# Performance work log

Hardware: AMD Instinct MI355X
Metric: run time of the kernel (lower is better)

The kernel has to match this reference:

```python
import jax, jax.numpy as jnp
import numpy as np

LN_EPS = 1e-5
CLAMP = 1e-8


def _linear(x, W, b):
    return x @ W + b


def _layernorm(x, g, b):
    mu = x.mean(-1, keepdims=True)
    var = ((x - mu) ** 2).mean(-1, keepdims=True)
    return (x - mu) / jnp.sqrt(var + LN_EPS) * g + b


def _residual(x, W1, b1, W2, b2):
    return jax.nn.relu(_linear(jax.nn.relu(_linear(x, W1, b1)), W2, b2)) + x


def _forward(node_emb, attn_Wq, attn_bq, attn_Wk, attn_bk, attn_Wv, attn_bv,
             attn_Wd, attn_bd, attn_ln_g, attn_ln_b,
             mlp_r1_w1, mlp_r1_b1, mlp_r1_w2, mlp_r1_b2,
             mlp_r2_w1, mlp_r2_b1, mlp_r2_w2, mlp_r2_b2,
             mlp_out_w, mlp_out_b,
             log_phi_r0, log_phi_r1h, log_phi_r1v, log_phi_r2, r0_idx, n):
    x = node_emb  # [1, n^2, D]
    L = attn_Wq.shape[0]
    for l in range(L):  # mask in the original is all zeros -> plain softmax attention
        q = _linear(x, attn_Wq[l], attn_bq[l])
        k = _linear(x, attn_Wk[l], attn_bk[l])
        v = _linear(x, attn_Wv[l], attn_bv[l])
        probs = jax.nn.softmax(jnp.einsum('bqd,bkd->bqk', q, k), axis=-1)
        ctx = jnp.einsum('bqk,bkd->bqd', probs, v)
        x = _layernorm(_linear(ctx, attn_Wd[l], attn_bd[l]) + x, attn_ln_g[l], attn_ln_b[l])
    x0 = x[0]                                  # [n^2, D]
    feats = x0[r0_idx].reshape(r0_idx.shape[0], -1)  # [R0, 4D]
    h = _residual(feats, mlp_r1_w1, mlp_r1_b1, mlp_r1_w2, mlp_r1_b2)
    h = _residual(h, mlp_r2_w1, mlp_r2_b1, mlp_r2_w2, mlp_r2_b2)
    logits = _linear(h, mlp_out_w, mlp_out_b)  # [R0, 16]
    beliefs = jax.nn.softmax(logits, axis=-1).reshape(-1, 2, 2, 2, 2)

    m = n - 1  # plaquettes per row
    # --- R1 horizontal interior edges (row r in 1..n-2, col c in 0..n-2) ---
    r, c = np.meshgrid(np.arange(1, n - 1), np.arange(m), indexing='ij')
    above = ((r - 1) * m + c).ravel()
    below = (r * m + c).ravel()
    h_stack = jnp.stack([beliefs[above].sum((1, 2)),   # edge nodes at plaquette pos 2,3
                         beliefs[below].sum((3, 4))])  # edge nodes at plaquette pos 0,1
    h_bel = h_stack.mean(0)                            # [Eh,2,2]
    mism = jnp.sum((h_stack - h_bel) ** 2)
    # --- R1 vertical interior edges (row r in 0..n-2, col c in 1..n-2) ---
    r, c = np.meshgrid(np.arange(m), np.arange(1, n - 1), indexing='ij')
    left = (r * m + (c - 1)).ravel()
    right = (r * m + c).ravel()
    v_stack = jnp.stack([beliefs[left].sum((1, 3)),    # edge nodes at pos 1,3
                         beliefs[right].sum((2, 4))])  # edge nodes at pos 0,2
    v_bel = v_stack.mean(0)                            # [Ev,2,2]
    mism = mism + jnp.sum((v_stack - v_bel) ** 2)
    # --- R2 interior nodes (r, c in 1..n-2), parents are the 4 incident edges ---
    r, c = np.meshgrid(np.arange(1, n - 1), np.arange(1, n - 1), indexing='ij')
    hl = ((r - 1) * m + (c - 1)).ravel()
    hr = ((r - 1) * m + c).ravel()
    vu = ((r - 1) * (n - 2) + (c - 1)).ravel()
    vd = (r * (n - 2) + (c - 1)).ravel()
    n_stack = jnp.stack([h_bel[hl].sum(1), h_bel[hr].sum(2),
                         v_bel[vu].sum(1), v_bel[vd].sum(2)])
    n_bel = n_stack.mean(0)                            # [V,2]
    mism = mism + jnp.sum((n_stack - n_bel) ** 2)

    # --- Kikuchi energy: counts +1 (plaquette), -1 (edge), +1 (node); log_phi detached ---
    def reg_energy(b, lphi, cnt):
        bc = jnp.maximum(b, CLAMP)
        return cnt * jnp.sum(bc * (jnp.log(bc) - jax.lax.stop_gradient(lphi)))

    energy = (reg_energy(beliefs, log_phi_r0, 1.0)
              + reg_energy(h_bel, log_phi_r1h, -1.0)
              + reg_energy(v_bel, log_phi_r1v, -1.0)
              + reg_energy(n_bel, log_phi_r2, 1.0))
    return energy, mism


def setup_inputs() -> dict:
    n, D, L, HID, OUT = 64, 256, 2, 1024, 16
    m = n - 1
    R0, E, V = m * m, (n - 2) * m, (n - 2) * (n - 2)
    key = jax.random.key(0)
    ks = jax.random.split(key, 24)
    norm = lambda k, sh, s=0.05: jax.random.normal(k, sh, dtype=jnp.float32) * s
    r, c = np.meshgrid(np.arange(m), np.arange(m), indexing='ij')
    i = (r * n + c).ravel()
    r0_idx = jnp.asarray(np.stack([i, i + 1, i + n, i + n + 1], 1), dtype=jnp.int32)
    inp = {
        'node_emb': jax.random.normal(ks[0], (1, n * n, D), dtype=jnp.float32),
        'attn_Wq': norm(ks[1], (L, D, D)), 'attn_bq': jnp.zeros((L, D), jnp.float32),
        'attn_Wk': norm(ks[2], (L, D, D)), 'attn_bk': jnp.zeros((L, D), jnp.float32),
        'attn_Wv': norm(ks[3], (L, D, D)), 'attn_bv': jnp.zeros((L, D), jnp.float32),
        'attn_Wd': norm(ks[4], (L, D, D)), 'attn_bd': jnp.zeros((L, D), jnp.float32),
        'attn_ln_g': jnp.ones((L, D), jnp.float32), 'attn_ln_b': jnp.zeros((L, D), jnp.float32),
        'mlp_r1_w1': norm(ks[5], (HID, HID), 0.03), 'mlp_r1_b1': jnp.zeros((HID,), jnp.float32),
        'mlp_r1_w2': norm(ks[6], (HID, HID), 0.03), 'mlp_r1_b2': jnp.zeros((HID,), jnp.float32),
        'mlp_r2_w1': norm(ks[7], (HID, HID), 0.03), 'mlp_r2_b1': jnp.zeros((HID,), jnp.float32),
        'mlp_r2_w2': norm(ks[8], (HID, HID), 0.03), 'mlp_r2_b2': jnp.zeros((HID,), jnp.float32),
        'mlp_out_w': norm(ks[9], (HID, OUT), 0.03), 'mlp_out_b': jnp.zeros((OUT,), jnp.float32),
        'log_phi_r0': jax.random.normal(ks[10], (R0, 2, 2, 2, 2), dtype=jnp.float32),
        'log_phi_r1h': jax.random.normal(ks[11], (E, 2, 2), dtype=jnp.float32),
        'log_phi_r1v': jax.random.normal(ks[12], (E, 2, 2), dtype=jnp.float32),
        'log_phi_r2': jax.random.normal(ks[13], (V, 2), dtype=jnp.float32),
        'r0_idx': r0_idx,
        'n': n,
    }
    return inp


def reference(node_emb, attn_Wq, attn_bq, attn_Wk, attn_bk, attn_Wv, attn_bv,
              attn_Wd, attn_bd, attn_ln_g, attn_ln_b,
              mlp_r1_w1, mlp_r1_b1, mlp_r1_w2, mlp_r1_b2,
              mlp_r2_w1, mlp_r2_b1, mlp_r2_w2, mlp_r2_b2,
              mlp_out_w, mlp_out_b,
              log_phi_r0, log_phi_r1h, log_phi_r1v, log_phi_r2, r0_idx, n):
    return _forward(node_emb, attn_Wq, attn_bq, attn_Wk, attn_bk, attn_Wv, attn_bv,
                    attn_Wd, attn_bd, attn_ln_g, attn_ln_b,
                    mlp_r1_w1, mlp_r1_b1, mlp_r1_w2, mlp_r1_b2,
                    mlp_r2_w1, mlp_r2_b1, mlp_r2_w2, mlp_r2_b2,
                    mlp_out_w, mlp_out_b,
                    log_phi_r0, log_phi_r1h, log_phi_r1v, log_phi_r2, r0_idx, n)
```

## Files before the change

### kernel.cpp

```cpp
#include <hip/hip_runtime.h>
#include <hip/hip_bf16.h>
#include <math.h>

#define D_    256
#define NSQ   4096
#define NL    2
#define HID_  1024
#define R0_   3969
#define EH_   3906
#define EV_   3906
#define NV_   3844
#define LN_EPS_ 1e-5f
#define CLAMP_  1e-8f
#define TK_    64

typedef float f32x4 __attribute__((ext_vector_type(4)));
typedef __bf16 bf16x8 __attribute__((ext_vector_type(8)));
typedef unsigned short u16x8 __attribute__((ext_vector_type(8)));

__device__ __forceinline__ void gload_lds16(const void* g, void* l) {
    __builtin_amdgcn_global_load_lds(
        (const __attribute__((address_space(1))) void*)g,
        (__attribute__((address_space(3))) void*)l, 16, 0, 0);
}

template<int BM, int BN>
__device__ __forceinline__ void gemm_body(
    const __hip_bfloat16* __restrict__ A, const __hip_bfloat16* __restrict__ Bt,
    const float* __restrict__ bias,
    const float* __restrict__ resf, const __hip_bfloat16* __restrict__ resb,
    void* __restrict__ C, int M, int N, int K, int relu, int outmode,
    int bx, int by)
{
    constexpr int WR  = BM / 64;
    constexpr int WC  = 4 / WR;
    constexpr int WNT = BN / WC;
    constexpr int NF  = WNT / 16;
    constexpr int ACH = BM / 64;
    constexpr int BCH = BN / 64;
    constexpr int ASZ = BM * 32;

    __shared__ __hip_bfloat16 sm[2][(BM + BN) * 32];

    const int t = threadIdx.x;
    const int lane = t & 63, wave = t >> 6;
    const int ln = lane & 15, lg = lane >> 4;
    const int wr = (WR == 1) ? 0 : (wave >> 1);
    const int wc = (WR == 1) ? wave : (wave & 1);
    const int row0 = bx * BM, col0 = by * BN;

    int aoff[ACH], boff[BCH];
    #pragma unroll
    for (int c = 0; c < ACH; ++c) {
        int e = (c * 256 + t) * 8;
        int row = e >> 5, slot = (e >> 3) & 3;
        int kg = slot ^ (row & 3) ^ ((row >> 2) & 3);
        aoff[c] = row * K + kg * 8;
    }
    #pragma unroll
    for (int c = 0; c < BCH; ++c) {
        int e = (c * 256 + t) * 8;
        int row = e >> 5, slot = (e >> 3) & 3;
        int kg = slot ^ (row & 3) ^ ((row >> 2) & 3);
        boff[c] = row * K + kg * 8;
    }
    const int sw = (ln & 3) ^ ((ln >> 2) & 3);

    const __hip_bfloat16* Ab = A + (size_t)row0 * K;
    const __hip_bfloat16* Bb = Bt + (size_t)col0 * K;

    f32x4 acc[4][NF];
    #pragma unroll
    for (int m = 0; m < 4; ++m)
        #pragma unroll
        for (int n = 0; n < NF; ++n) acc[m][n] = f32x4{0.f, 0.f, 0.f, 0.f};

    auto STAGE = [&](int k0, int buf) {
        #pragma unroll
        for (int c = 0; c < ACH; ++c)
            gload_lds16(Ab + k0 + aoff[c], (char*)&sm[buf][0] + (c * 256 + t) * 16);
        #pragma unroll
        for (int c = 0; c < BCH; ++c)
            gload_lds16(Bb + k0 + boff[c], (char*)&sm[buf][ASZ] + (c * 256 + t) * 16);
    };

    STAGE(0, 0);
    __syncthreads();
    int cur = 0;
    for (int k0 = 0; k0 < K; k0 += 32) {
        if (k0 + 32 < K) STAGE(k0 + 32, cur ^ 1);
        bf16x8 af[4], bfr[NF];
        #pragma unroll
        for (int m = 0; m < 4; ++m)
            af[m] = *(const bf16x8*)((const char*)&sm[cur][0] +
                     (size_t)(wr * 64 + m * 16 + ln) * 64 + ((lg ^ sw) << 4));
        #pragma unroll
        for (int n = 0; n < NF; ++n)
            bfr[n] = *(const bf16x8*)((const char*)&sm[cur][ASZ] +
                     (size_t)(wc * WNT + n * 16 + ln) * 64 + ((lg ^ sw) << 4));
        #pragma unroll
        for (int m = 0; m < 4; ++m)
            #pragma unroll
            for (int n = 0; n < NF; ++n)
                acc[m][n] = __builtin_amdgcn_mfma_f32_16x16x32_bf16(
                    af[m], bfr[n], acc[m][n], 0, 0, 0);
        __syncthreads();
        cur ^= 1;
    }

    #pragma unroll
    for (int m = 0; m < 4; ++m) {
        const int rowb = row0 + wr * 64 + m * 16 + lg * 4;
        #pragma unroll
        for (int n = 0; n < NF; ++n) {
            const int col = col0 + wc * WNT + n * 16 + ln;
            const float bv = bias ? bias[col] : 0.f;
            if (outmode == 2) {
                union { ushort4 u4; __hip_bfloat16 h[4]; } pk;
                #pragma unroll
                for (int r = 0; r < 4; ++r) {
                    float v = acc[m][n][r] + bv;
                    if (relu) v = fmaxf(v, 0.f);
                    pk.h[r] = __float2bfloat16(v);
                }
                *(ushort4*)((__hip_bfloat16*)C + (size_t)col * M + rowb) = pk.u4;
            } else if (outmode == 3) {
                union { ushort4 u4; __hip_bfloat16 h[4]; } pk;
                #pragma unroll
                for (int r = 0; r < 4; ++r) {
                    float v = acc[m][n][r] + bv;
                    if (relu) v = fmaxf(v, 0.f);
                    pk.h[r] = __float2bfloat16(v);
                }
                size_t off = ((size_t)((rowb >> 5) * 16 + (col >> 4)) << 9)
                           + (size_t)(((rowb >> 3) & 3) * 16 + (col & 15)) * 8
                           + (rowb & 7);
                *(ushort4*)((__hip_bfloat16*)C + off) = pk.u4;
            } else {
                #pragma unroll
                for (int r = 0; r < 4; ++r) {
                    float v = acc[m][n][r] + bv;
                    if (relu) v = fmaxf(v, 0.f);
                    const size_t idx = (size_t)(rowb + r) * N + col;
                    if (resf) v += resf[idx];
                    if (resb) v += __bfloat162float(resb[idx]);
                    if (outmode == 0) ((float*)C)[idx] = v;
                    else ((__hip_bfloat16*)C)[idx] = __float2bfloat16(v);
                }
            }
        }
    }
}

template<int BM, int BN>
__global__ __launch_bounds__(256) void gemm_t(
    const __hip_bfloat16* __restrict__ A, const __hip_bfloat16* __restrict__ Bt,
    const float* __restrict__ bias,
    const float* __restrict__ resf, const __hip_bfloat16* __restrict__ resb,
    void* __restrict__ C, int M, int N, int K, int relu, int outmode)
{
    gemm_body<BM, BN>(A, Bt, bias, resf, resb, C, M, N, K, relu, outmode,
                      blockIdx.x, blockIdx.y);
}

__global__ __launch_bounds__(256) void gemm_qkv(
    const __hip_bfloat16* __restrict__ xb,
    const __hip_bfloat16* __restrict__ wqkt2, const __hip_bfloat16* __restrict__ wvt2,
    const float* __restrict__ bqk2, const float* __restrict__ bv,
    __hip_bfloat16* __restrict__ qkb, __hip_bfloat16* __restrict__ vf, int l)
{
    const __hip_bfloat16* Bt;
    const float* bias;
    void* C;
    int N, outmode, by;
    if (blockIdx.y < 8) {
        Bt = wqkt2 + (size_t)l * 131072; bias = bqk2 + l * 512;
        C = qkb; N = 512; outmode = 1; by = blockIdx.y;
    } else {
        Bt = wvt2 + (size_t)l * 65536; bias = bv + l * D_;
        C = vf; N = D_; outmode = 3; by = blockIdx.y - 8;
    }
    gemm_body<64, 64>(xb, Bt, bias, nullptr, nullptr, C, NSQ, N, D_, 0, outmode,
                      blockIdx.x, by);
}

__global__ __launch_bounds__(256) void gemm_n16b(
    const __hip_bfloat16* __restrict__ A, const __hip_bfloat16* __restrict__ Bt,
    const float* __restrict__ bias, const float* __restrict__ lphi0,
    float* __restrict__ beliefs, float* __restrict__ out, int M, int K)
{
    const int t = threadIdx.x, lane = t & 63, wave = t >> 6;
    const int ln = lane & 15, lg = lane >> 4;
    const int r0 = blockIdx.x * 64 + wave * 16;
    f32x4 acc = {0.f, 0.f, 0.f, 0.f};
    for (int k0 = 0; k0 < K; k0 += 32) {
        bf16x8 a = *(const bf16x8*)(A + (size_t)(r0 + ln) * K + k0 + lg * 8);
        bf16x8 b = *(const bf16x8*)(Bt + (size_t)ln * K + k0 + lg * 8);
        acc = __builtin_amdgcn_mfma_f32_16x16x32_bf16(a, b, acc, 0, 0, 0);
    }
    float e = 0.f;
    #pragma unroll
    for (int r = 0; r < 4; ++r) {
        const int row = r0 + lg * 4 + r;
        float v = acc[r] + bias[ln];
        float mx = v;
        mx = fmaxf(mx, __shfl_xor(mx, 1));
        mx = fmaxf(mx, __shfl_xor(mx, 2));
        mx = fmaxf(mx, __shfl_xor(mx, 4));
        mx = fmaxf(mx, __shfl_xor(mx, 8));
        float ex = __expf(v - mx);
        float s = ex;
        s += __shfl_xor(s, 1);
        s += __shfl_xor(s, 2);
        s += __shfl_xor(s, 4);
        s += __shfl_xor(s, 8);
        if (row < R0_) {
            float bb = ex / s;
            beliefs[(size_t)row * 16 + ln] = bb;
            float bc = fmaxf(bb, CLAMP_);
            e += bc * (logf(bc) - lphi0[(size_t)row * 16 + ln]);
        }
    }
    #pragma unroll
    for (int off = 32; off; off >>= 1) e += __shfl_down(e, off);
    if (lane == 0) atomicAdd(&out[0], e);
}

__global__ __launch_bounds__(256) void prep_k(
    const float* __restrict__ node_emb, __hip_bfloat16* __restrict__ xb,
    const float* __restrict__ outw, __hip_bfloat16* __restrict__ outwt,
    const float* __restrict__ Wq, const float* __restrict__ Wk,
    const float* __restrict__ Wv, const float* __restrict__ Wd,
    __hip_bfloat16* __restrict__ wqkt2, __hip_bfloat16* __restrict__ wvt2,
    __hip_bfloat16* __restrict__ wdt2,
    const float* __restrict__ bq, const float* __restrict__ bk,
    float* __restrict__ bqk2,
    const float* __restrict__ M0, const float* __restrict__ M1,
    const float* __restrict__ M2, const float* __restrict__ M3,
    __hip_bfloat16* __restrict__ T0, __hip_bfloat16* __restrict__ T1,
    __hip_bfloat16* __restrict__ T2, __hip_bfloat16* __restrict__ T3)
{
    __shared__ float tile[32][33];
    const int b = blockIdx.x, t = threadIdx.x;
    if (b < 1024) {
        int p = b * 256 + t;
        float4 v = *(const float4*)(node_emb + (size_t)p * 4);
        union { ushort4 u4; __hip_bfloat16 h[4]; } pk;
        pk.h[0] = __float2bfloat16(v.x); pk.h[1] = __float2bfloat16(v.y);
        pk.h[2] = __float2bfloat16(v.z); pk.h[3] = __float2bfloat16(v.w);
        *(ushort4*)(xb + (size_t)p * 4) = pk.u4;
    } else if (b < 1088) {
        int i = (b - 1024) * 256 + t;
        int n = i >> 10, k = i & 1023;
        outwt[i] = __float2bfloat16(outw[k * 16 + n]);
    } else if (b < 1600) {
        int idx = b - 1088;
        int z = idx >> 6, bx = (idx >> 3) & 7, by = idx & 7;
        int l = z >> 2, w = z & 3;
        const float* W = (w == 0 ? Wq : w == 1 ? Wk : w == 2 ? Wv : Wd) + (size_t)l * 65536;
        __hip_bfloat16* Wt = w == 0 ? wqkt2 + (size_t)l * 131072
                           : w == 1 ? wqkt2 + (size_t)l * 131072 + 65536
                           : w == 2 ? wvt2 + (size_t)l * 65536
                                    : wdt2 + (size_t)l * 65536;
        int k0 = bx * 32, n0 = by * 32;
        int r = t >> 3, c4 = (t & 7) * 4;
        float4 v = *(const float4*)(W + (size_t)(k0 + r) * 256 + n0 + c4);
        tile[r][c4 + 0] = v.x; tile[r][c4 + 1] = v.y;
        tile[r][c4 + 2] = v.z; tile[r][c4 + 3] = v.w;
        __syncthreads();
        union { ushort4 u4; __hip_bfloat16 h[4]; } pk;
        #pragma unroll
        for (int i = 0; i < 4; ++i) pk.h[i] = __float2bfloat16(tile[c4 + i][r]);
        *(ushort4*)(Wt + (size_t)(n0 + r) * 256 + k0 + c4) = pk.u4;
    } else if (b < 1604) {
        int idx = (b - 1600) * 256 + t;
        int l = idx >> 9, j = idx & 511;
        bqk2[idx] = j < 256 ? bq[l * 256 + j] : bk[l * 256 + j - 256];
    } else {
        int idx = b - 1604;
        int z = idx >> 10, rem = idx & 1023;
        const float* W = z == 0 ? M0 : z == 1 ? M1 : z == 2 ? M2 : M3;
        __hip_bfloat16* Wt = z == 0 ? T0 : z == 1 ? T1 : z == 2 ? T2 : T3;
        int k0 = (rem >> 5) * 32, n0 = (rem & 31) * 32;
        int r = t >> 3, c4 = (t & 7) * 4;
        float4 v = *(const float4*)(W + (size_t)(k0 + r) * 1024 + n0 + c4);
        tile[r][c4 + 0] = v.x; tile[r][c4 + 1] = v.y;
        tile[r][c4 + 2] = v.z; tile[r][c4 + 3] = v.w;
        __syncthreads();
        union { ushort4 u4; __hip_bfloat16 h[4]; } pk;
        #pragma unroll
        for (int i = 0; i < 4; ++i) pk.h[i] = __float2bfloat16(tile[c4 + i][r]);
        *(ushort4*)(Wt + (size_t)(n0 + r) * 1024 + k0 + c4) = pk.u4;
    }
}

template<int KS>
__global__ __launch_bounds__(512, 2) void attn_mfma_t(
    const __hip_bfloat16* __restrict__ qk, const __hip_bfloat16* __restrict__ vf,
    __hip_bfloat16* __restrict__ po, float* __restrict__ pm, float* __restrict__ pl)
{
    constexpr int KRANGE = NSQ / KS;
    constexpr int NT = KRANGE / TK_;
    constexpr int VOFF = 65536;
    constexpr int POFF = 98304;
    const int t = threadIdx.x;
    const int wave = t >> 6, lane = t & 63;
    const int ln = lane & 15, lg = lane >> 4;
    const int q0 = blockIdx.x * 128 + wave * 16;
    const int ks = blockIdx.y;
    const int k0 = ks * KRANGE;

    __shared__ __align__(16) char smem[116736];

    bf16x8 qa[8];
    #pragma unroll
    for (int s = 0; s < 8; ++s)
        qa[s] = *(const bf16x8*)(qk + (size_t)(q0 + ln) * 512 + s * 32 + lg * 8);

    int srcoff[4];
    #pragma unroll
    for (int c = 0; c < 4; ++c) {
        int row = c * 16 + (t >> 5);
        int g = (t & 31) ^ ((row & 15) << 1);
        srcoff[c] = row * 512 + 256 + g * 8;
    }
    int rb[8];
    #pragma unroll
    for (int s8 = 0; s8 < 8; ++s8)
        rb[s8] = ln * 512 + (((s8 * 4 + lg) ^ (ln << 1)) << 4);

    f32x4 o[16];
    #pragma unroll
    for (int nt = 0; nt < 16; ++nt) o[nt] = f32x4{0.f, 0.f, 0.f, 0.f};
    float rm = -1e30f, rl = 0.f;

    {
        const __hip_bfloat16* src = qk + (size_t)k0 * 512;
        #pragma unroll
        for (int c = 0; c < 4; ++c)
            gload_lds16(src + srcoff[c], smem + c * 8192 + t * 16);
    }
    __syncthreads();

    for (int it = 0; it < NT; ++it) {
        const int cur = it & 1;
        {
            const __hip_bfloat16* vsrc = vf + ((size_t)((k0 + it * TK_) >> 5) << 13);
            #pragma unroll
            for (int c = 0; c < 4; ++c) {
                int idx = c * 512 + t;
                gload_lds16(vsrc + (size_t)idx * 8, smem + VOFF + idx * 16);
            }
        }
        {
            const int itn = (it + 1 < NT) ? it + 1 : it;
            const __hip_bfloat16* src = qk + (size_t)(k0 + itn * TK_) * 512;
            #pragma unroll
            for (int c = 0; c < 4; ++c)
                gload_lds16(src + srcoff[c], smem + (cur ^ 1) * 32768 + c * 8192 + t * 16);
        }
        const char* kbase = smem + cur * 32768;
        f32x4 s4[4];
        #pragma unroll
        for (int nt = 0; nt < 4; ++nt) {
            f32x4 acc = {0.f, 0.f, 0.f, 0.f};
            #pragma unroll
            for (int s8 = 0; s8 < 8; ++s8) {
                bf16x8 kb = *(const bf16x8*)(kbase + nt * 8192 + rb[s8]);
                acc = __builtin_amdgcn_mfma_f32_16x16x32_bf16(kb, qa[s8], acc, 0, 0, 0);
            }
            s4[nt] = acc;
        }
        float mx = -1e30f;
        #pragma unroll
        for (int nt = 0; nt < 4; ++nt)
            #pragma unroll
            for (int r = 0; r < 4; ++r) mx = fmaxf(mx, s4[nt][r]);
        mx = fmaxf(mx, __shfl_xor(mx, 16));
        mx = fmaxf(mx, __shfl_xor(mx, 32));
        float sc = 1.f;
        if (__any(mx > rm + 8.f)) {
            float mnew = fmaxf(rm, mx);
            sc = __expf(rm - mnew);
            rm = mnew;
            float scr[4];
            #pragma unroll
            for (int r = 0; r < 4; ++r) scr[r] = __shfl(sc, lg * 4 + r);
            #pragma unroll
            for (int nt = 0; nt < 16; ++nt)
                #pragma unroll
                for (int r = 0; r < 4; ++r) o[nt][r] *= scr[r];
        }
        float rs = 0.f;
        #pragma unroll
        for (int nt = 0; nt < 4; ++nt)
            #pragma unroll
            for (int r = 0; r < 4; ++r) {
                float p = __expf(s4[nt][r] - rm);
                s4[nt][r] = p;
                rs += p;
            }
        rs += __shfl_xor(rs, 16);
        rs += __shfl_xor(rs, 32);
        rl = rl * sc + rs;
        char* prow = smem + POFF + wave * 2304 + ln * 144;
        #pragma unroll
        for (int nt = 0; nt < 4; ++nt) {
            union { ushort4 u4; __hip_bfloat16 h[4]; } pk;
            #pragma unroll
            for (int r = 0; r < 4; ++r) pk.h[r] = __float2bfloat16(s4[nt][r]);
            *(ushort4*)(prow + nt * 32 + lg * 8) = pk.u4;
        }
        asm volatile("s_waitcnt lgkmcnt(0)" ::: "memory");
        __builtin_amdgcn_sched_barrier(0);
        bf16x8 pa0 = *(const bf16x8*)(prow + lg * 16);
        bf16x8 pa1 = *(const bf16x8*)(prow + 64 + lg * 16);
        asm volatile("s_waitcnt vmcnt(4)" ::: "memory");
        __builtin_amdgcn_sched_barrier(0);
        __builtin_amdgcn_s_barrier();
        const char* vl = smem + VOFF;
        #pragma unroll
        for (int ntd = 0; ntd < 16; ++ntd) {
            bf16x8 vb0 = *(const bf16x8*)(vl + ntd * 1024 + lane * 16);
            bf16x8 vb1 = *(const bf16x8*)(vl + 16384 + ntd * 1024 + lane * 16);
            o[ntd] = __builtin_amdgcn_mfma_f32_16x16x32_bf16(pa0, vb0, o[ntd], 0, 0, 0);
            o[ntd] = __builtin_amdgcn_mfma_f32_16x16x32_bf16(pa1, vb1, o[ntd], 0, 0, 0);
        }
        __syncthreads();
    }
    unsigned short* ob = (unsigned short*)(smem + wave * 8448);
    #pragma unroll
    for (int nt = 0; nt < 16; ++nt)
        #pragma unroll
        for (int r = 0; r < 4; ++r) {
            __hip_bfloat16 h = __float2bfloat16(o[nt][r]);
            ob[(lg * 4 + r) * 264 + nt * 16 + ln] = *(unsigned short*)&h;
        }
    asm volatile("s_waitcnt lgkmcnt(0)" ::: "memory");
    __builtin_amdgcn_sched_barrier(0);
    unsigned short* pob = (unsigned short*)po;
    #pragma unroll
    for (int i = 0; i < 8; ++i) {
        int f = i * 64 + lane;
        int row = f >> 5, dc = f & 31;
        u16x8 vv = *(const u16x8*)(ob + row * 264 + dc * 8);
        *(u16x8*)(pob + ((size_t)ks * NSQ + q0 + row) * D_ + dc * 8) = vv;
    }
    if (lane < 16) {
        pm[ks * NSQ + q0 + lane] = rm;
        pl[ks * NSQ + q0 + lane] = rl;
    }
}

template<int KS>
__global__ __launch_bounds__(256) void attn_combine_t(
    const __hip_bfloat16* __restrict__ po, const float* __restrict__ pm,
    const float* __restrict__ pl, __hip_bfloat16* __restrict__ ctx)
{
    const int idx8 = blockIdx.x * 256 + threadIdx.x;
    const int row = idx8 >> 5;
    float m[KS], ms = -1e30f;
    #pragma unroll
    for (int s = 0; s < KS; ++s) { m[s] = pm[s * NSQ + row]; ms = fmaxf(ms, m[s]); }
    float l = 0.f, w[KS];
    #pragma unroll
    for (int s = 0; s < KS; ++s) {
        w[s] = __expf(m[s] - ms);
        l += w[s] * pl[s * NSQ + row];
    }
    const float inv = 1.f / l;
    float num[8];
    #pragma unroll
    for (int j = 0; j < 8; ++j) num[j] = 0.f;
    #pragma unroll
    for (int s = 0; s < KS; ++s) {
        u16x8 v = *(const u16x8*)(po + (size_t)s * (NSQ * D_) + (size_t)idx8 * 8);
        #pragma unroll
        for (int j = 0; j < 8; ++j) {
            union { float f; unsigned u; } cv;
            cv.u = (unsigned)v[j] << 16;
            num[j] += w[s] * cv.f;
        }
    }
    union { u16x8 u8; __hip_bfloat16 h[8]; } pk;
    #pragma unroll
    for (int j = 0; j < 8; ++j) pk.h[j] = __float2bfloat16(num[j] * inv);
    *(u16x8*)(ctx + (size_t)idx8 * 8) = pk.u8;
}

__global__ __launch_bounds__(256) void ln_f32(
    const float* __restrict__ y, const float* __restrict__ g,
    const float* __restrict__ b, float* __restrict__ xo,
    __hip_bfloat16* __restrict__ xob, __hip_bfloat16* __restrict__ feats, int fin)
{
    const int lane = threadIdx.x & 63, wave = threadIdx.x >> 6;
    const int row = blockIdx.x * 4 + wave;
    float4 v = *(const float4*)(y + (size_t)row * D_ + lane * 4);
    float s = v.x + v.y + v.z + v.w;
    #pragma unroll
    for (int off = 1; off < 64; off <<= 1) s += __shfl_xor(s, off);
    float mu = s * (1.f / D_);
    float dx = v.x - mu, dy = v.y - mu, dz = v.z - mu, dw = v.w - mu;
    float q = dx * dx + dy * dy + dz * dz + dw * dw;
    #pragma unroll
    for (int off = 1; off < 64; off <<= 1) q += __shfl_xor(q, off);
    float inv = rsqrtf(q * (1.f / D_) + LN_EPS_);
    float4 gg = *(const float4*)(g + lane * 4);
    float4 bb = *(const float4*)(b + lane * 4);
    float4 o;
    o.x = dx * inv * gg.x + bb.x;
    o.y = dy * inv * gg.y + bb.y;
    o.z = dz * inv * gg.z + bb.z;
    o.w = dw * inv * gg.w + bb.w;
    union { ushort4 u4; __hip_bfloat16 h[4]; } pk;
    pk.h[0] = __float2bfloat16(o.x); pk.h[1] = __float2bfloat16(o.y);
    pk.h[2] = __float2bfloat16(o.z); pk.h[3] = __float2bfloat16(o.w);
    if (!fin) {
        *(float4*)(xo + (size_t)row * D_ + lane * 4) = o;
        *(ushort4*)(xob + (size_t)row * D_ + lane * 4) = pk.u4;
    } else {
        const int r = row >> 6, c = row & 63;
        if (r < 63 && c < 63)
            *(ushort4*)(feats + (size_t)(r * 63 + c) * 1024 + lane * 4) = pk.u4;
        if (r < 63 && c > 0)
            *(ushort4*)(feats + (size_t)(r * 63 + c - 1) * 1024 + 256 + lane * 4) = pk.u4;
        if (r > 0 && c < 63)
            *(ushort4*)(feats + (size_t)((r - 1) * 63 + c) * 1024 + 512 + lane * 4) = pk.u4;
        if (r > 0 && c > 0)
            *(ushort4*)(feats + (size_t)((r - 1) * 63 + c - 1) * 1024 + 768 + lane * 4) = pk.u4;
    }
}

__global__ __launch_bounds__(256) void edges_k(
    const float* __restrict__ beliefs, const float* __restrict__ lphih,
    const float* __restrict__ lphiv, float* __restrict__ hbel,
    float* __restrict__ vbel, float* __restrict__ out)
{
    int e = blockIdx.x * 256 + threadIdx.x;
    float el = 0.f, ml = 0.f;
    if (blockIdx.y == 0) {
        if (e < EH_) {
            const float* bA = beliefs + (size_t)e * 16;
            const float* bB = beliefs + (size_t)(e + 63) * 16;
            float s0[4] = {0,0,0,0}, s1[4] = {0,0,0,0};
            #pragma unroll
            for (int ab = 0; ab < 4; ++ab)
                #pragma unroll
                for (int cd = 0; cd < 4; ++cd) {
                    s0[cd] += bA[ab * 4 + cd];
                    s1[ab] += bB[ab * 4 + cd];
                }
            #pragma unroll
            for (int z = 0; z < 4; ++z) {
                float hb = 0.5f * (s0[z] + s1[z]);
                hbel[e * 4 + z] = hb;
                float d0 = s0[z] - hb, d1 = s1[z] - hb;
                ml += d0 * d0 + d1 * d1;
                float bc = fmaxf(hb, CLAMP_);
                el -= bc * (logf(bc) - lphih[e * 4 + z]);
            }
        }
    } else {
        if (e < EV_) {
            int r = e / 62, c = e % 62 + 1;
            const float* bL = beliefs + (size_t)(r * 63 + c - 1) * 16;
            const float* bR = beliefs + (size_t)(r * 63 + c) * 16;
            float s0[4] = {0,0,0,0}, s1[4] = {0,0,0,0};
            #pragma unroll
            for (int a = 0; a < 2; ++a)
                #pragma unroll
                for (int bq = 0; bq < 2; ++bq)
                    #pragma unroll
                    for (int c2 = 0; c2 < 2; ++c2)
                        #pragma unroll
                        for (int d = 0; d < 2; ++d) {
                            int idx = a * 8 + bq * 4 + c2 * 2 + d;
                            s0[bq * 2 + d]  += bL[idx];
                            s1[a * 2 + c2] += bR[idx];
                        }
            #pragma unroll
            for (int z = 0; z < 4; ++z) {
                float vb = 0.5f * (s0[z] + s1[z]);
                vbel[e * 4 + z] = vb;
                float d0 = s0[z] - vb, d1 = s1[z] - vb;
                ml += d0 * d0 + d1 * d1;
                float bc = fmaxf(vb, CLAMP_);
                el -= bc * (logf(bc) - lphiv[e * 4 + z]);
            }
        }
    }
    for (int off = 32; off; off >>= 1) { el += __shfl_down(el, off); ml += __shfl_down(ml, off); }
    if ((threadIdx.x & 63) == 0) { atomicAdd(&out[0], el); atomicAdd(&out[1], ml); }
}

__global__ __launch_bounds__(256) void node_k(
    const float* __restrict__ hbel, const float* __restrict__ vbel,
    const float* __restrict__ lphi2, float* __restrict__ out)
{
    int vtx = blockIdx.x * 256 + threadIdx.x;
    float el = 0.f, ml = 0.f;
    if (vtx < NV_) {
        int hl = (vtx / 62) * 63 + (vtx % 62);
        int hr = hl + 1;
        int vu = vtx;
        int vd = vtx + 62;
        float n0[2], n1[2], n2[2], n3[2];
        #pragma unroll
        for (int z = 0; z < 2; ++z) {
            n0[z] = hbel[hl * 4 + z] + hbel[hl * 4 + 2 + z];
            n1[z] = hbel[hr * 4 + z * 2] + hbel[hr * 4 + z * 2 + 1];
            n2[z] = vbel[vu * 4 + z] + vbel[vu * 4 + 2 + z];
            n3[z] = vbel[vd * 4 + z * 2] + vbel[vd * 4 + z * 2 + 1];
        }
        #pragma unroll
        for (int z = 0; z < 2; ++z) {
            float nb = 0.25f * (n0[z] + n1[z] + n2[z] + n3[z]);
            float d0 = n0[z] - nb, d1 = n1[z] - nb, d2 = n2[z] - nb, d3 = n3[z] - nb;
            ml += d0 * d0 + d1 * d1 + d2 * d2 + d3 * d3;
            float bc = fmaxf(nb, CLAMP_);
            el += bc * (logf(bc) - lphi2[vtx * 2 + z]);
        }
    }
    for (int off = 32; off; off >>= 1) { el += __shfl_down(el, off); ml += __shfl_down(ml, off); }
    if ((threadIdx.x & 63) == 0) { atomicAdd(&out[0], el); atomicAdd(&out[1], ml); }
}

extern "C" void kernel_launch(void* const* d_in, const int* in_sizes, int n_in,
                              void* d_out, int out_size, void* d_ws, size_t ws_size,
                              hipStream_t stream)
{
    (void)in_sizes; (void)n_in; (void)out_size; (void)ws_size;
    const float* node_emb = (const float*)d_in[0];
    const float* Wq  = (const float*)d_in[1];
    const float* bq  = (const float*)d_in[2];
    const float* Wk  = (const float*)d_in[3];
    const float* bk  = (const float*)d_in[4];
    const float* Wv  = (const float*)d_in[5];
    const float* bv  = (const float*)d_in[6];
    const float* Wd  = (const float*)d_in[7];
    const float* bd  = (const float*)d_in[8];
    const float* lng = (const float*)d_in[9];
    const float* lnb = (const float*)d_in[10];
    const float* r1w1 = (const float*)d_in[11];
    const float* r1b1 = (const float*)d_in[12];
    const float* r1w2 = (const float*)d_in[13];
    const float* r1b2 = (const float*)d_in[14];
    const float* r2w1 = (const float*)d_in[15];
    const float* r2b1 = (const float*)d_in[16];
    const float* r2w2 = (const float*)d_in[17];
    const float* r2b2 = (const float*)d_in[18];
    const float* outw = (const float*)d_in[19];
    const float* outb = (const float*)d_in[20];
    const float* lphi0 = (const float*)d_in[21];
    const float* lphih = (const float*)d_in[22];
    const float* lphiv = (const float*)d_in[23];
    const float* lphi2 = (const float*)d_in[24];

    float* ws = (float*)d_ws;
    float* x      = ws;
    __hip_bfloat16* xb = (__hip_bfloat16*)(ws + 1048576);
    float* belief = ws + 1638400;
    float* hbel   = ws + 1703936;
    float* vbel   = ws + 1720320;
    __hip_bfloat16* outwt = (__hip_bfloat16*)(ws + 1736704);
    float* arena  = ws + 1744896;

    __hip_bfloat16* wqkt2 = (__hip_bfloat16*)(arena);
    __hip_bfloat16* wvt2  = (__hip_bfloat16*)(arena + 131072);
    __hip_bfloat16* wdt2  = (__hip_bfloat16*)(arena + 196608);
    float* bqk2 = arena + 262144;
    __hip_bfloat16* qkb = (__hip_bfloat16*)(arena + 263168);
    __hip_bfloat16* vf  = (__hip_bfloat16*)(arena + 1311744);
    __hip_bfloat16* ctxb = vf;
    float* yb = arena + 1836032;
    float* pm = arena + 2884608;
    float* pl = arena + 2950144;
    __hip_bfloat16* po = (__hip_bfloat16*)(arena + 3015680);

    __hip_bfloat16* feats = (__hip_bfloat16*)(ws + 8954880);
    __hip_bfloat16* w1t = (__hip_bfloat16*)(ws + 11052032);
    __hip_bfloat16* w2t = (__hip_bfloat16*)(ws + 11576320);
    __hip_bfloat16* w3t = (__hip_bfloat16*)(ws + 12100608);
    __hip_bfloat16* w4t = (__hip_bfloat16*)(ws + 12624896);
    __hip_bfloat16* hA  = (__hip_bfloat16*)(arena);
    __hip_bfloat16* hB  = (__hip_bfloat16*)(arena + 2097152);

    hipMemsetAsync(d_out, 0, 2 * sizeof(float), stream);

    dim3 blk(256);
    dim3 blk512(512);
    prep_k<<<dim3(5700), blk, 0, stream>>>(node_emb, xb, outw, outwt,
                                           Wq, Wk, Wv, Wd, wqkt2, wvt2, wdt2,
                                           bq, bk, bqk2,
                                           r1w1, r1w2, r2w1, r2w2,
                                           w1t, w2t, w3t, w4t);

    for (int l = 0; l < NL; ++l) {
        gemm_qkv<<<dim3(64, 12), blk, 0, stream>>>(xb, wqkt2, wvt2, bqk2, bv,
                                                   qkb, vf, l);
        attn_mfma_t<8><<<dim3(NSQ / 128, 8), blk512, 0, stream>>>(qkb, vf, po, pm, pl);
        attn_combine_t<8><<<dim3(NSQ * D_ / 2048), blk, 0, stream>>>(po, pm, pl, ctxb);
        gemm_t<64, 64><<<dim3(NSQ / 64, D_ / 64), blk, 0, stream>>>(
            ctxb, wdt2 + (size_t)l * 65536, bd + l * D_,
            (l == 0 ? node_emb : x), nullptr, yb, NSQ, D_, D_, 0, 0);
        ln_f32<<<dim3(NSQ / 4), blk, 0, stream>>>(yb, lng + l * D_, lnb + l * D_,
                                                  x, xb, feats, l);
    }

    dim3 gM(NSQ / 64, HID_ / 128);
    gemm_t<64, 128><<<gM, blk, 0, stream>>>(feats, w1t, r1b1, nullptr, nullptr,
                                            hA, NSQ, HID_, HID_, 1, 1);
    gemm_t<64, 128><<<gM, blk, 0, stream>>>(hA, w2t, r1b2, nullptr, feats,
                                            hB, NSQ, HID_, HID_, 1, 1);
    gemm_t<64, 128><<<gM, blk, 0, stream>>>(hB, w3t, r2b1, nullptr, nullptr,
                                            hA, NSQ, HID_, HID_, 1, 1);
    gemm_t<64, 128><<<gM, blk, 0, stream>>>(hA, w4t, r2b2, nullptr, hB,
                                            feats, NSQ, HID_, HID_, 1, 1);

    float* outp = (float*)d_out;
    gemm_n16b<<<dim3(NSQ / 64), blk, 0, stream>>>(feats, outwt, outb, lphi0,
                                                  belief, outp, NSQ, HID_);
    edges_k<<<dim3((EH_ + 255) / 256, 2), blk, 0, stream>>>(belief, lphih, lphiv,
                                                            hbel, vbel, outp);
    node_k<<<dim3((NV_ + 255) / 256), blk, 0, stream>>>(hbel, vbel, lphi2, outp);
}
```

Before: 241.7 us.

## Add 128x128 double-buffered MLP GEMM and widen QKV tiles

```diff
diff --git a/kernel.cpp b/kernel.cpp
--- a/kernel.cpp
+++ b/kernel.cpp
@@ -173,15 +173,90 @@
     const float* bias;
     void* C;
     int N, outmode, by;
-    if (blockIdx.y < 8) {
+    if (blockIdx.y < 4) {
         Bt = wqkt2 + (size_t)l * 131072; bias = bqk2 + l * 512;
         C = qkb; N = 512; outmode = 1; by = blockIdx.y;
     } else {
         Bt = wvt2 + (size_t)l * 65536; bias = bv + l * D_;
-        C = vf; N = D_; outmode = 3; by = blockIdx.y - 8;
-    }
-    gemm_body<64, 64>(xb, Bt, bias, nullptr, nullptr, C, NSQ, N, D_, 0, outmode,
-                      blockIdx.x, by);
+        C = vf; N = D_; outmode = 3; by = blockIdx.y - 4;
+    }
+    gemm_body<64, 128>(xb, Bt, bias, nullptr, nullptr, C, NSQ, N, D_, 0, outmode,
+                       blockIdx.x, by);
+}
+
+__global__ __launch_bounds__(512, 4) void gemm_128(
+    const __hip_bfloat16* __restrict__ A, const __hip_bfloat16* __restrict__ Bt,
+    const float* __restrict__ bias, const __hip_bfloat16* __restrict__ resb,
+    __hip_bfloat16* __restrict__ C, int M, int N, int K, int relu)
+{
+    __shared__ __hip_bfloat16 sm[2][8192];
+
+    const int t = threadIdx.x;
+    const int lane = t & 63, wave = t >> 6;
+    const int ln = lane & 15, lg = lane >> 4;
+    const int wr = wave >> 2, wc = wave & 3;
+    const int row0 = blockIdx.x * 128, col0 = blockIdx.y * 128;
+
+    const int srow = t >> 2, sslot = t & 3;
+    const int skg = sslot ^ (srow & 3) ^ ((srow >> 2) & 3);
+    const int soff = srow * K + skg * 8;
+    const int sw = (ln & 3) ^ ((ln >> 2) & 3);
+
+    const __hip_bfloat16* Ab = A + (size_t)row0 * K;
+    const __hip_bfloat16* Bb = Bt + (size_t)col0 * K;
+
+    f32x4 acc[4][2];
+    #pragma unroll
+    for (int m = 0; m < 4; ++m)
+        #pragma unroll
+        for (int n = 0; n < 2; ++n) acc[m][n] = f32x4{0.f, 0.f, 0.f, 0.f};
+
+    auto STAGE = [&](int k0, int buf) {
+        gload_lds16(Ab + k0 + soff, (char*)&sm[buf][0] + t * 16);
+        gload_lds16(Bb + k0 + soff, (char*)&sm[buf][4096] + t * 16);
+    };
+
+    STAGE(0, 0);
+    __syncthreads();
+    int cur = 0;
+    for (int k0 = 0; k0 < K; k0 += 32) {
+        if (k0 + 32 < K) STAGE(k0 + 32, cur ^ 1);
+        bf16x8 af[4], bfr[2];
+        #pragma unroll
+        for (int m = 0; m < 4; ++m)
+            af[m] = *(const bf16x8*)((const char*)&sm[cur][0] +
+                     (size_t)(wr * 64 + m * 16 + ln) * 64 + ((lg ^ sw) << 4));
+        #pragma unroll
+        for (int n = 0; n < 2; ++n)
+            bfr[n] = *(const bf16x8*)((const char*)&sm[cur][4096] +
+                     (size_t)(wc * 32 + n * 16 + ln) * 64 + ((lg ^ sw) << 4));
+        #pragma unroll
+        for (int m = 0; m < 4; ++m)
+            #pragma unroll
+            for (int n = 0; n < 2; ++n)
+                acc[m][n] = __builtin_amdgcn_mfma_f32_16x16x32_bf16(
+                    af[m], bfr[n], acc[m][n], 0, 0, 0);
+        __syncthreads();
+        cur ^= 1;
+    }
+
+    #pragma unroll
+    for (int m = 0; m < 4; ++m) {
+        const int rowb = row0 + wr * 64 + m * 16 + lg * 4;
+        #pragma unroll
+        for (int n = 0; n < 2; ++n) {
+            const int col = col0 + wc * 32 + n * 16 + ln;
+            const float bv = bias[col];
+            #pragma unroll
+            for (int r = 0; r < 4; ++r) {
+                float v = acc[m][n][r] + bv;
+                if (relu) v = fmaxf(v, 0.f);
+                const size_t idx = (size_t)(rowb + r) * N + col;
+                if (resb) v += __bfloat162float(resb[idx]);
+                C[idx] = __float2bfloat16(v);
+            }
+        }
+    }
 }
 
 __global__ __launch_bounds__(256) void gemm_n16b(
@@ -696,8 +771,8 @@
                                            w1t, w2t, w3t, w4t);
 
     for (int l = 0; l < NL; ++l) {
-        gemm_qkv<<<dim3(64, 12), blk, 0, stream>>>(xb, wqkt2, wvt2, bqk2, bv,
-                                                   qkb, vf, l);
+        gemm_qkv<<<dim3(64, 6), blk, 0, stream>>>(xb, wqkt2, wvt2, bqk2, bv,
+                                                  qkb, vf, l);
         attn_mfma_t<8><<<dim3(NSQ / 128, 8), blk512, 0, stream>>>(qkb, vf, po, pm, pl);
         attn_combine_t<8><<<dim3(NSQ * D_ / 2048), blk, 0, stream>>>(po, pm, pl, ctxb);
         gemm_t<64, 64><<<dim3(NSQ / 64, D_ / 64), blk, 0, stream>>>(
@@ -707,15 +782,15 @@
                                                   x, xb, feats, l);
     }
 
-    dim3 gM(NSQ / 64, HID_ / 128);
-    gemm_t<64, 128><<<gM, blk, 0, stream>>>(feats, w1t, r1b1, nullptr, nullptr,
-                                            hA, NSQ, HID_, HID_, 1, 1);
-    gemm_t<64, 128><<<gM, blk, 0, stream>>>(hA, w2t, r1b2, nullptr, feats,
-                                            hB, NSQ, HID_, HID_, 1, 1);
-    gemm_t<64, 128><<<gM, blk, 0, stream>>>(hB, w3t, r2b1, nullptr, nullptr,
-                                            hA, NSQ, HID_, HID_, 1, 1);
-    gemm_t<64, 128><<<gM, blk, 0, stream>>>(hA, w4t, r2b2, nullptr, hB,
-                                            feats, NSQ, HID_, HID_, 1, 1);
+    dim3 gM(NSQ / 128, HID_ / 128);
+    gemm_128<<<gM, blk512, 0, stream>>>(feats, w1t, r1b1, nullptr,
+                                        hA, NSQ, HID_, HID_, 1);
+    gemm_128<<<gM, blk512, 0, stream>>>(hA, w2t, r1b2, feats,
+                                        hB, NSQ, HID_, HID_, 1);
+    gemm_128<<<gM, blk512, 0, stream>>>(hB, w3t, r2b1, nullptr,
+                                        hA, NSQ, HID_, HID_, 1);
+    gemm_128<<<gM, blk512, 0, stream>>>(hA, w4t, r2b2, hB,
+                                        feats, NSQ, HID_, HID_, 1);
 
     float* outp = (float*)d_out;
     gemm_n16b<<<dim3(NSQ / 64), blk, 0, stream>>>(feats, outwt, outb, lphi0,
```

Result: no change. 238.1 us (-1.5%).
